# Kernel optimization log

Hardware: AMD Instinct MI355X
Metric: run time of the kernel (lower is better)

The kernel has to match this reference:

```python
import jax, jax.numpy as jnp
import numpy as np
from math import factorial

B, C, D = 1024, 10, 16
EPS = 1e-07


def _moment_weights(dim, order):
    # weight[idx] = prod(multiplicity!)/order!  (de-duplicates symmetric index tuples)
    if order == 1:
        return np.ones((dim,), dtype=np.float32)
    grids = np.meshgrid(*([np.arange(dim)] * order), indexing='ij')
    idx = np.stack(grids, axis=-1)  # [dim]*order + [order]
    prodm = np.ones(idx.shape[:-1], dtype=np.float64)
    for p in range(order):
        r = np.ones(idx.shape[:-1], dtype=np.float64)
        for q in range(p):
            r += (idx[..., q] == idx[..., p])
        prodm *= r  # running multiplicities multiply to prod(m!)
    return (prodm / float(factorial(order))).astype(np.float32)


def _gauss_moments(dim, order):
    # joint moments of N(0, I) via Isserlis' theorem
    eye = np.eye(dim)
    if order == 1:
        return np.zeros((dim,), np.float32)
    if order == 2:
        return eye.astype(np.float32)
    if order == 3:
        return np.zeros((dim, dim, dim), np.float32)
    g = (np.einsum('ij,kl->ijkl', eye, eye)
         + np.einsum('ik,jl->ijkl', eye, eye)
         + np.einsum('il,jk->ijkl', eye, eye))
    return g.astype(np.float32)


def _sroot(x, c1, p, c2):
    # signed compressive root: sign(sign(x)+0.1) * ((|x|+c1)^p - c2)
    return jnp.sign(jnp.sign(x) + 0.1) * (jnp.power(jnp.abs(x) + c1, p) - c2)


def setup_inputs() -> dict:
    key = jax.random.key(0)
    k1, k2, k3 = jax.random.split(key, 3)
    return {
        'embedding': jax.random.normal(k1, (B, D), dtype=jnp.float32),
        'centers': jax.random.normal(k2, (C, D), dtype=jnp.float32),
        'logits': jax.random.normal(k3, (B, C), dtype=jnp.float32),
        'gm1': jnp.asarray(_gauss_moments(D, 1)),
        'gm2': jnp.asarray(_gauss_moments(D, 2)),
        'gm3': jnp.asarray(_gauss_moments(D, 3)),
        'gm4': jnp.asarray(_gauss_moments(D, 4)),
        'mw1': jnp.asarray(_moment_weights(D, 1)),
        'mw2': jnp.asarray(_moment_weights(D, 2)),
        'mw3': jnp.asarray(_moment_weights(D, 3)),
        'mw4': jnp.asarray(_moment_weights(D, 4)),
    }


def reference(embedding, centers, logits, gm1, gm2, gm3, gm4, mw1, mw2, mw3, mw4):
    num_classes = logits.shape[1]
    assign = jnp.argmax(logits, axis=-1)                      # [B]
    onehot = jax.nn.one_hot(assign, num_classes, dtype=embedding.dtype)  # [B,C]
    diff = embedding[:, None, :] - centers[None, :, :]        # [B,C,D]
    d = diff * onehot[:, :, None]                             # diff_onehot [B,C,D]
    cw = jnp.sum(onehot, axis=0)                              # cluster_weight [C]

    # fused moment contractions (original materializes [B,C,D^k] then sums over B;
    # onehot is 0/1 so onehot^k == onehot -> identical math)
    m1 = jnp.sum(d, axis=0) / (cw[:, None] + EPS)                             # [C,D]
    m2 = jnp.einsum('bci,bcj->cij', d, d) / (cw[:, None, None] + EPS)         # [C,D,D]
    m3 = jnp.einsum('bci,bcj,bck->cijk', d, d, d)                             # [C,D,D,D] (no count division, as in original)
    m4 = jnp.einsum('bci,bcj,bck,bcl->cijkl', d, d, d, d)                     # [C,D,D,D,D]

    m2 = _sroot(m2, 0.25, 0.5, 0.5)
    m3 = _sroot(m3, 0.19245008973, 0.3333333333, 0.57735026919)
    m4 = _sroot(m4, 0.15749013123, 0.25, 0.62996052494)
    t1 = gm1
    t2 = _sroot(gm2, 0.25, 0.5, 0.5)
    t3 = _sroot(gm3, 0.19245008973, 0.3333333333, 0.57735026919)
    t4 = _sroot(gm4, 0.15749013123, 0.25, 0.62996052494)

    cwn = cw / jnp.sum(cw)                                     # [C]
    w1 = cwn[:, None] * mw1[None, :]
    w2 = cwn[:, None, None] * mw2[None]
    w3 = cwn[:, None, None, None] * mw3[None]
    w4 = cwn[:, None, None, None, None] * mw4[None]

    p1 = jnp.sum(w1 * jnp.square(m1 - t1[None]))
    p2 = jnp.sum(w2 * jnp.square(m2 - t2[None]))
    p3 = jnp.sum(w3 * jnp.square(m3 - t3[None]))
    p4 = jnp.sum(w4 * jnp.square(m4 - t4[None]))
    return 1.0 * p1 + 0.5 * p2 + 0.25 * p3 + 0.125 * p4
```

## Files before the change

kernel.cpp:

```cpp
#include <hip/hip_runtime.h>
#include <math.h>

#define BN 1024
#define CN 10
#define DN 16
#define NE1 16
#define NE2 136
#define NE3 816
#define NE4 3876
#define NENT 4844
#define EB 19
#define CH 256
#define EPSV 1e-7f

__device__ __forceinline__ int H2f(int n){ return n*(n+1)/2; }
__device__ __forceinline__ int H3f(int n){ return n*(n+1)*(n+2)/6; }

__device__ __forceinline__ float sroot2f(float x){
  float s = (x<0.f)?-1.f:1.f;
  return s*(sqrtf(fabsf(x)+0.25f)-0.5f);
}
__device__ __forceinline__ float sroot3f(float x){
  float s=(x<0.f)?-1.f:1.f;
  return s*(cbrtf(fabsf(x)+0.19245008973f)-0.57735026919f);
}
__device__ __forceinline__ float sroot4f(float x){
  float s=(x<0.f)?-1.f:1.f;
  return s*(sqrtf(sqrtf(fabsf(x)+0.15749013123f))-0.62996052494f);
}

__global__ __launch_bounds__(256) void kb(
    const float* __restrict__ emb, const float* __restrict__ centers,
    const float* __restrict__ logits,
    const float* __restrict__ gm1, const float* __restrict__ gm2,
    const float* __restrict__ gm3, const float* __restrict__ gm4,
    float* __restrict__ out) {
  __shared__ float sx[17][CH+1];
  __shared__ float red[256];
  __shared__ int   memb[BN];
  __shared__ int   wcnt[4][4];
  int tid  = threadIdx.x;
  int lane = tid & 63;
  int wave = tid >> 6;
  int c  = blockIdx.x / EB;
  int eb = blockIdx.x % EB;

  for (int n=tid; n<CH+1; n+=256) sx[16][n] = 1.f;

  int rank_r[4]; bool match_r[4];
  #pragma unroll
  for (int r=0;r<4;r++) {
    int b = r*256 + tid;
    const float* lr = logits + b*CN;
    float best = lr[0]; int bi = 0;
    #pragma unroll
    for (int q=1;q<CN;q++){ float v=lr[q]; if (v>best){best=v;bi=q;} }
    unsigned long long m = __ballot(bi==c);
    match_r[r] = (bi==c);
    rank_r[r] = __popcll(m & ((1ull<<lane)-1ull));
    if (lane==0) wcnt[r][wave] = __popcll(m);
  }
  __syncthreads();
  int pre[17]; pre[0]=0;
  #pragma unroll
  for (int p=0;p<16;p++) pre[p+1] = pre[p] + wcnt[p>>2][p&3];
  int cnt = pre[16];
  #pragma unroll
  for (int r=0;r<4;r++)
    if (match_r[r]) memb[pre[r*4+wave] + rank_r[r]] = r*256 + tid;

  int e = eb*256 + tid;
  int ii=16, jj=16, kk=16, ll=16, order=1;
  float tg = 0.f;
  bool valid = (e < NENT);
  if (valid) {
    if (e < NE1) {
      order=1; ii=e;
      tg = gm1[ii];
    } else if (e < NE1+NE2) {
      order=2; int r = e-NE1;
      int i=0; while (r >= DN-i){ r -= DN-i; i++; }
      ii=i; jj=i+r;
      tg = sroot2f(gm2[ii*DN+jj]);
    } else if (e < NE1+NE2+NE3) {
      order=3; int r = e-(NE1+NE2);
      int i=0; while (r >= H2f(DN-i)){ r -= H2f(DN-i); i++; }
      int j=i; while (r >= DN-j){ r -= DN-j; j++; }
      ii=i; jj=j; kk=j+r;
      tg = sroot3f(gm3[(ii*DN+jj)*DN+kk]);
    } else {
      order=4; int r = e-(NE1+NE2+NE3);
      int i=0; while (r >= H3f(DN-i)){ r -= H3f(DN-i); i++; }
      int j=i; while (r >= H2f(DN-j)){ r -= H2f(DN-j); j++; }
      int k=j; while (r >= DN-k){ r -= DN-k; k++; }
      ii=i; jj=j; kk=k; ll=k+r;
      tg = sroot4f(gm4[((ii*DN+jj)*DN+kk)*DN+ll]);
    }
  }

  float mom = 0.f;
  for (int base=0; base<cnt; base+=CH) {
    int m = min(CH, cnt-base);
    __syncthreads();
    if (tid < m) {
      int b = memb[base + tid];
      const float4* er = (const float4*)(emb + b*DN);
      const float4* cr = (const float4*)(centers + c*DN);
      float4 e0=er[0], e1=er[1], e2=er[2], e3=er[3];
      float4 c0=cr[0], c1=cr[1], c2=cr[2], c3=cr[3];
      float v[16];
      v[0]=e0.x-c0.x; v[1]=e0.y-c0.y; v[2]=e0.z-c0.z; v[3]=e0.w-c0.w;
      v[4]=e1.x-c1.x; v[5]=e1.y-c1.y; v[6]=e1.z-c1.z; v[7]=e1.w-c1.w;
      v[8]=e2.x-c2.x; v[9]=e2.y-c2.y; v[10]=e2.z-c2.z; v[11]=e2.w-c2.w;
      v[12]=e3.x-c3.x; v[13]=e3.y-c3.y; v[14]=e3.z-c3.z; v[15]=e3.w-c3.w;
      #pragma unroll
      for (int i=0;i<16;i++) sx[i][tid] = v[i];
    }
    __syncthreads();
    for (int n=0; n<m; n++) {
      mom += sx[ii][n]*sx[jj][n]*sx[kk][n]*sx[ll][n];
    }
  }

  float contrib = 0.f;
  if (valid) {
    float mval = mom;
    if (order <= 2) mval /= ((float)cnt + EPSV);
    float v;
    if      (order==1) v = mval - tg;
    else if (order==2) v = sroot2f(mval) - tg;
    else if (order==3) v = sroot3f(mval) - tg;
    else               v = sroot4f(mval) - tg;
    float lw = (order==1)?1.f:(order==2)?0.5f:(order==3)?0.25f:0.125f;
    float cwn = (float)cnt * (1.f/1024.f);
    contrib = lw * cwn * v * v;
  }

  red[tid] = contrib;
  __syncthreads();
  for (int s=128; s>0; s>>=1) {
    if (tid < s) red[tid] += red[tid+s];
    __syncthreads();
  }
  if (tid==0) atomicAdd(out, red[0]);
}

extern "C" void kernel_launch(void* const* d_in, const int* in_sizes, int n_in,
                              void* d_out, int out_size, void* d_ws, size_t ws_size,
                              hipStream_t stream) {
  const float* emb  = (const float*)d_in[0];
  const float* cen  = (const float*)d_in[1];
  const float* logi = (const float*)d_in[2];
  const float* gm1  = (const float*)d_in[3];
  const float* gm2  = (const float*)d_in[4];
  const float* gm3  = (const float*)d_in[5];
  const float* gm4  = (const float*)d_in[6];

  hipMemsetAsync(d_out, 0, sizeof(float), stream);
  kb<<<CN*EB, 256, 0, stream>>>(emb, cen, logi, gm1, gm2, gm3, gm4, (float*)d_out);
}
```

Before: 18.99 us.

## Vectorize moment inner loop with float4 LDS reads and order-specialized paths

Replaces the padded ones-row trick with order-specialized inner loops that read four samples at a time via float4 shared-memory loads, padding each chunk to a multiple of four with zeros. It also moves the membership scatter after index decoding to overlap latency, and swaps the shared-memory tree reduction for a wave shuffle reduction. The aim is to cut LDS instruction count and wasted multiplies for lower-order moments. Branches diverge across order boundaries within a wave, and the padding writes add a small serial step.

```diff
diff --git a/kernel.cpp b/kernel.cpp
--- a/kernel.cpp
+++ b/kernel.cpp
@@ -11,6 +11,7 @@
 #define NENT 4844
 #define EB 19
 #define CH 256
+#define SST 260
 #define EPSV 1e-7f
 
 __device__ __forceinline__ int H2f(int n){ return n*(n+1)/2; }
@@ -35,17 +36,15 @@
     const float* __restrict__ gm1, const float* __restrict__ gm2,
     const float* __restrict__ gm3, const float* __restrict__ gm4,
     float* __restrict__ out) {
-  __shared__ float sx[17][CH+1];
-  __shared__ float red[256];
+  __shared__ float sx[DN][SST];
   __shared__ int   memb[BN];
   __shared__ int   wcnt[4][4];
+  __shared__ float wred[4];
   int tid  = threadIdx.x;
   int lane = tid & 63;
   int wave = tid >> 6;
   int c  = blockIdx.x / EB;
   int eb = blockIdx.x % EB;
-
-  for (int n=tid; n<CH+1; n+=256) sx[16][n] = 1.f;
 
   int rank_r[4]; bool match_r[4];
   #pragma unroll
@@ -60,17 +59,9 @@
     rank_r[r] = __popcll(m & ((1ull<<lane)-1ull));
     if (lane==0) wcnt[r][wave] = __popcll(m);
   }
-  __syncthreads();
-  int pre[17]; pre[0]=0;
-  #pragma unroll
-  for (int p=0;p<16;p++) pre[p+1] = pre[p] + wcnt[p>>2][p&3];
-  int cnt = pre[16];
-  #pragma unroll
-  for (int r=0;r<4;r++)
-    if (match_r[r]) memb[pre[r*4+wave] + rank_r[r]] = r*256 + tid;
 
   int e = eb*256 + tid;
-  int ii=16, jj=16, kk=16, ll=16, order=1;
+  int ii=0, jj=0, kk=0, ll=0, order=0;
   float tg = 0.f;
   bool valid = (e < NENT);
   if (valid) {
@@ -98,9 +89,24 @@
     }
   }
 
+  __syncthreads();
+  int pre[17]; pre[0]=0;
+  #pragma unroll
+  for (int p=0;p<16;p++) pre[p+1] = pre[p] + wcnt[p>>2][p&3];
+  int cnt = pre[16];
+  #pragma unroll
+  for (int r=0;r<4;r++)
+    if (match_r[r]) memb[pre[r*4+wave] + rank_r[r]] = r*256 + tid;
+
+  const float* pA = &sx[ii][0];
+  const float* pB = &sx[jj][0];
+  const float* pC = &sx[kk][0];
+  const float* pD = &sx[ll][0];
+
   float mom = 0.f;
   for (int base=0; base<cnt; base+=CH) {
-    int m = min(CH, cnt-base);
+    int m  = min(CH, cnt-base);
+    int mp = (m+3)&~3;
     __syncthreads();
     if (tid < m) {
       int b = memb[base + tid];
@@ -114,11 +120,34 @@
       v[8]=e2.x-c2.x; v[9]=e2.y-c2.y; v[10]=e2.z-c2.z; v[11]=e2.w-c2.w;
       v[12]=e3.x-c3.x; v[13]=e3.y-c3.y; v[14]=e3.z-c3.z; v[15]=e3.w-c3.w;
       #pragma unroll
-      for (int i=0;i<16;i++) sx[i][tid] = v[i];
+      for (int i=0;i<DN;i++) sx[i][tid] = v[i];
     }
+    if (tid < DN)
+      for (int n=m; n<mp; n++) sx[tid][n] = 0.f;
     __syncthreads();
-    for (int n=0; n<m; n++) {
-      mom += sx[ii][n]*sx[jj][n]*sx[kk][n]*sx[ll][n];
+    if (order==4) {
+      for (int n=0; n<mp; n+=4) {
+        float4 a=*(const float4*)(pA+n), b=*(const float4*)(pB+n);
+        float4 cc=*(const float4*)(pC+n), d=*(const float4*)(pD+n);
+        mom += a.x*b.x*cc.x*d.x + a.y*b.y*cc.y*d.y
+             + a.z*b.z*cc.z*d.z + a.w*b.w*cc.w*d.w;
+      }
+    } else if (order==3) {
+      for (int n=0; n<mp; n+=4) {
+        float4 a=*(const float4*)(pA+n), b=*(const float4*)(pB+n);
+        float4 cc=*(const float4*)(pC+n);
+        mom += a.x*b.x*cc.x + a.y*b.y*cc.y + a.z*b.z*cc.z + a.w*b.w*cc.w;
+      }
+    } else if (order==2) {
+      for (int n=0; n<mp; n+=4) {
+        float4 a=*(const float4*)(pA+n), b=*(const float4*)(pB+n);
+        mom += a.x*b.x + a.y*b.y + a.z*b.z + a.w*b.w;
+      }
+    } else if (order==1) {
+      for (int n=0; n<mp; n+=4) {
+        float4 a=*(const float4*)(pA+n);
+        mom += a.x + a.y + a.z + a.w;
+      }
     }
   }
 
@@ -136,13 +165,11 @@
     contrib = lw * cwn * v * v;
   }
 
-  red[tid] = contrib;
+  #pragma unroll
+  for (int off=32; off; off>>=1) contrib += __shfl_down(contrib, off, 64);
+  if (lane==0) wred[wave] = contrib;
   __syncthreads();
-  for (int s=128; s>0; s>>=1) {
-    if (tid < s) red[tid] += red[tid+s];
-    __syncthreads();
-  }
-  if (tid==0) atomicAdd(out, red[0]);
+  if (tid==0) atomicAdd(out, wred[0]+wred[1]+wred[2]+wred[3]);
 }
 
 extern "C" void kernel_launch(void* const* d_in, const int* in_sizes, int n_in,
```

Result: faster. 18.11 us (-4.6%).
